# Kernel optimization log

Hardware: AMD Instinct MI355X
Metric: run time of the kernel (lower is better)

The kernel has to match this reference:

```python
import jax, jax.numpy as jnp
import numpy as np

BN_EPS = 1e-5


def _conv1x1(x, W, b):
    # x: (B, Cin, H, W), W: (Cout, Cin), b: (Cout,)
    return jnp.einsum('bchw,oc->bohw', x, W) + b[None, :, None, None]


def _bn(x, gamma, beta, mean, var):
    # inference-mode BatchNorm2d with running stats
    inv = gamma / jnp.sqrt(var + BN_EPS)
    return x * inv[None, :, None, None] + (beta - mean * inv)[None, :, None, None]


def setup_inputs() -> dict:
    key = jax.random.key(0)
    ks = jax.random.split(key, 8)
    B, N, C, H, W = 4, 3, 256, 48, 48
    Ck = C // 2  # key/query/value channels (scale=2)
    s = 0.02
    return {
        'x': jax.random.normal(ks[0], (B, N, C, H, W), jnp.float32),
        # f_key / f_query (shared): conv1x1 + BN
        'Wk': jax.random.normal(ks[1], (Ck, C), jnp.float32) * s,
        'bk': jnp.zeros((Ck,), jnp.float32),
        'gk': jnp.ones((Ck,), jnp.float32),
        'betak': jnp.zeros((Ck,), jnp.float32),
        'mk': jnp.zeros((Ck,), jnp.float32),
        'vk': jnp.ones((Ck,), jnp.float32),
        # f_value
        'Wv': jax.random.normal(ks[2], (Ck, C), jnp.float32) * s,
        'bv': jnp.zeros((Ck,), jnp.float32),
        # f_out
        'Wo': jax.random.normal(ks[3], (C, Ck), jnp.float32) * s,
        'bo': jnp.zeros((C,), jnp.float32),
        # fuse_layer: in = 2*C, out = C
        'Wf': jax.random.normal(ks[4], (C, 2 * C), jnp.float32) * s,
        'bf': jnp.zeros((C,), jnp.float32),
    }


def reference(x, Wk, bk, gk, betak, mk, vk, Wv, bv, Wo, bo, Wf, bf):
    B, N, C, H, W = x.shape  # N == 3
    HW = H * W
    Ck = Wk.shape[0]
    scale = Ck ** (-0.5)

    # Precompute shared key/query and value features for all 3 views
    xf = x.reshape(B * N, C, H, W)
    k_all = _bn(_conv1x1(xf, Wk, bk), gk, betak, mk, vk).reshape(B, N, Ck, HW)
    v_all = _conv1x1(xf, Wv, bv).reshape(B, N, Ck, HW)

    outs = []
    attn_maps = []
    for i in range(3):  # fixed small structural loop over views
        adj_ids = [j for j in range(3) if j != i]
        ref = x[:, i]                          # (B, C, H, W)
        q = k_all[:, i].transpose(0, 2, 1)     # (B, HW, Ck)  f_query == f_key
        matching = jnp.zeros_like(ref)
        for j in adj_ids:
            sim = jnp.einsum('bqc,bck->bqk', q, k_all[:, j]) * scale  # (B, HW, HW)
            attn = jax.nn.softmax(sim, axis=-1)
            ctx = jnp.einsum('bqk,bck->bcq', attn, v_all[:, j])       # (B, Ck, HW)
            ctx = ctx.reshape(B, Ck, H, W)
            matching = matching + _conv1x1(ctx, Wo, bo)
            if i == 0:
                attn_maps.append(attn)
        fuse = _conv1x1(jnp.concatenate([ref, matching], axis=1), Wf, bf)
        outs.append(ref + fuse)

    out = jnp.stack(outs, axis=1)                    # (B, 3, C, H, W)
    attention_maps = jnp.stack(attn_maps, axis=1)    # (B, 2, HW, HW)
    return out, attention_maps
```

## Files before the change

### kernel.cpp

```cpp
#include <hip/hip_runtime.h>

typedef short s8v __attribute__((ext_vector_type(8)));
typedef short s4v __attribute__((ext_vector_type(4)));
typedef float f4v __attribute__((ext_vector_type(4)));
typedef unsigned u32v2 __attribute__((ext_vector_type(2)));
typedef unsigned short u16;

#define MFMA(a,b,c) __builtin_amdgcn_mfma_f32_16x16x32_bf16(a,b,c,0,0,0)

__device__ __forceinline__ float bf2f(u16 x){
  unsigned u = ((unsigned)x) << 16;
  return __builtin_bit_cast(float, u);
}
__device__ __forceinline__ u16 f2bf(float f){
  unsigned u = __builtin_bit_cast(unsigned, f);
  u += 0x7FFFu + ((u >> 16) & 1u);
  return (u16)(u >> 16);
}

__device__ __forceinline__ void gload16(const void* g, void* l){
  __builtin_amdgcn_global_load_lds((const __attribute__((address_space(1))) unsigned*)g,
                                   (__attribute__((address_space(3))) unsigned*)l, 16, 0, 0);
}
__device__ __forceinline__ void nt_store4(float* p, f4v v){
  __builtin_nontemporal_store(v, (f4v*)p);
}

#define CC   256
#define CK   128
#define HW   2304
#define NF   12
#define C2E  0.1275174996992022f
#define OFF_KT   14155776u
#define OFF_V    21233664u
#define OFF_CTX  28311552u
#define OFF_RS   42467328u
#define OFF_PAR  42541056u
#define OFF_WK16 42543104u
#define OFF_WV16 42608640u
#define OFF_WF16 42674176u
#define OFF_WCMB 42936320u

__global__ void cv_weights(const float* __restrict__ Wk, const float* __restrict__ Wv,
                           const float* __restrict__ Wf,
                           u16* __restrict__ Wk16, u16* __restrict__ Wv16, u16* __restrict__ Wf16){
  int i = blockIdx.x*256 + threadIdx.x;
  if (i < 32768){ Wk16[i] = f2bf(Wk[i]); Wv16[i] = f2bf(Wv[i]); }
  Wf16[i] = f2bf(Wf[i]);
}

__global__ void k0_params(const float* __restrict__ bk, const float* __restrict__ gk,
                          const float* __restrict__ betak, const float* __restrict__ mk,
                          const float* __restrict__ vk, const float* __restrict__ Wo,
                          const float* __restrict__ Wf, const float* __restrict__ bo,
                          const float* __restrict__ bfv,
                          float* kscale, float* kbias, float* btot, u16* Wcomb){
  int c = blockIdx.x;
  int o = threadIdx.x;
  float acc = 0.f;
  for(int m=0;m<256;m++)
    acc += Wf[(size_t)o*512 + 256 + m] * Wo[(size_t)m*128 + c];
  Wcomb[(size_t)o*128 + c] = f2bf(acc);
  if (c == 0){
    float a2 = 0.f;
    for(int m=0;m<256;m++)
      a2 += Wf[(size_t)o*512 + 256 + m] * bo[m];
    btot[o] = bfv[o] + 2.0f*a2;
    if (o < 128){
      float inv = gk[o] * rsqrtf(vk[o] + 1e-5f);
      kscale[o] = inv;
      kbias[o]  = betak[o] + (bk[o] - mk[o])*inv;
    }
  }
}

__device__ __forceinline__ void stage_xt(const float* __restrict__ xf, int pb, int tid, char* xt){
  #pragma unroll
  for(int it=0; it<16; ++it){
    int idx = tid + 256*it;
    int c = idx>>4, slot = idx&15;
    f4v v = *(const f4v*)(xf + (size_t)c*HW + pb + slot*4);
    #pragma unroll
    for(int u=0;u<4;u++){
      int p = slot*4+u;
      *(u16*)(xt + p*512 + ((2*c) ^ ((p&7)<<4))) = f2bf(v[u]);
    }
  }
}
__device__ __forceinline__ s8v xt_frag(const char* xt, int r, int kt, int g){
  return *(const s8v*)(xt + r*512 + (((unsigned)(64*kt+16*g)) ^ ((unsigned)(r&7)<<4)));
}

__global__ __launch_bounds__(256) void k1_kv(const float* __restrict__ x, const u16* __restrict__ Wk,
                                             const u16* __restrict__ Wv, const float* __restrict__ bv,
                                             const float* __restrict__ kscale, const float* __restrict__ kbias,
                                             u16* __restrict__ kT, u16* __restrict__ vout){
  int f  = blockIdx.y;
  int pb = blockIdx.x*64;
  int tid = threadIdx.x;
  int w = tid>>6, l = tid&63, s = l&15, g = l>>4;
  __shared__ char xt[32768];
  stage_xt(x + (size_t)f*CC*HW, pb, tid, xt);
  __syncthreads();
  {
    s8v afr[8];
    #pragma unroll
    for(int kt=0;kt<8;kt++) afr[kt] = xt_frag(xt, 16*w+s, kt, g);
    f4v acc[8] = {};
    #pragma unroll
    for(int kt=0;kt<8;kt++){
      #pragma unroll
      for(int nt=0;nt<8;nt++){
        s8v b = *(const s8v*)(Wk + (size_t)(16*nt+s)*CC + 32*kt + 8*g);
        acc[nt] = MFMA(afr[kt], b, acc[nt]);
      }
    }
    u16* kout = kT + (size_t)f*HW*CK;
    int q0 = pb + 16*w;
    #pragma unroll
    for(int nt=0;nt<8;nt++){
      int o = 16*nt + s;
      float sc = kscale[o], bi = kbias[o];
      #pragma unroll
      for(int r=0;r<4;r++){
        int q = q0 + 4*g + r;
        kout[(size_t)q*CK + o] = f2bf(acc[nt][r]*sc + bi);
      }
    }
  }
  {
    s8v afr[2][8];
    #pragma unroll
    for(int mt=0;mt<2;mt++)
      #pragma unroll
      for(int kt=0;kt<8;kt++)
        afr[mt][kt] = *(const s8v*)(Wv + (size_t)(32*w+16*mt+s)*CC + 32*kt + 8*g);
    f4v acc[2][4] = {};
    #pragma unroll
    for(int kt=0;kt<8;kt++){
      #pragma unroll
      for(int nt=0;nt<4;nt++){
        s8v b = xt_frag(xt, 16*nt+s, kt, g);
        #pragma unroll
        for(int mt=0;mt<2;mt++)
          acc[mt][nt] = MFMA(afr[mt][kt], b, acc[mt][nt]);
      }
    }
    u16* vf = vout + (size_t)f*CK*HW;
    #pragma unroll
    for(int mt=0;mt<2;mt++){
      #pragma unroll
      for(int r=0;r<4;r++){
        int o = 32*w + 16*mt + 4*g + r;
        float bvo = bv[o];
        #pragma unroll
        for(int nt=0;nt<4;nt++)
          vf[(size_t)o*HW + pb + 16*nt + s] = f2bf(acc[mt][nt][r] + bvo);
      }
    }
  }
}

__global__ __launch_bounds__(256, 2) void k2_attn(const u16* __restrict__ kT, const u16* __restrict__ v,
                                                  u16* __restrict__ ctxS, float* __restrict__ rowsum_ws){
  int qb  = blockIdx.x;
  int bij = blockIdx.y;
  int b = bij/6, r6 = bij - 6*b, i = r6>>1, jj = r6&1;
  int adj0 = (i==0) ? 1 : 0;
  int adj1 = (i==2) ? 1 : 2;
  int j = jj ? adj1 : adj0;
  int tid = threadIdx.x;
  int w = tid>>6, l = tid&63, s = l&15, g = l>>4;
  int q0 = qb*128 + w*32;

  __shared__ char L[81920];
  char* plw = L + 65536 + w*4096;

  const u16* kTi = kT + (size_t)(b*3+i)*HW*CK;
  const u16* kTj = kT + (size_t)(b*3+j)*HW*CK;
  const u16* vj  = v  + (size_t)(b*3+j)*CK*HW;

  s8v qfr[2][4];
  #pragma unroll
  for(int qf=0;qf<2;qf++)
    #pragma unroll
    for(int kt=0;kt<4;kt++)
      qfr[qf][kt] = *(const s8v*)(kTi + (size_t)(q0+16*qf+s)*CK + 32*kt + 8*g);

  f4v ctx[8][2] = {};
  float psum[2] = {0.f, 0.f};

  auto STAGE = [&](int p0, int buf){
    const char* kbase = (const char*)kTj + (size_t)p0*256;
    const char* vbase = (const char*)vj  + (size_t)p0*2;
    char* lK = L + buf*16384 + w*1024;
    char* lV = L + 32768 + buf*16384 + w*1024;
    #pragma unroll
    for(int it=0; it<4; ++it){
      unsigned Lo = (unsigned)tid*16u + (unsigned)it*4096u;
      unsigned Gs = Lo ^ (((Lo>>8)&7u)<<4);
      gload16(kbase + Gs, lK + it*4096);
      unsigned row = Lo>>7;
      unsigned col = (Lo & 127u) ^ ((row&7u)<<4);
      gload16(vbase + (size_t)row*(HW*2) + col, lV + it*4096);
    }
  };

  STAGE(0, 0);
  __syncthreads();
  int cur = 0;

  for(int pt=0; pt<36; ++pt){
    if (pt < 35) STAGE((pt+1)*64, cur^1);
    const char* lK = L + cur*16384;
    const char* lV = L + 32768 + cur*16384;

    f4v sa[2][4] = {};
    __builtin_amdgcn_s_setprio(1);
    #pragma unroll
    for(int kt=0;kt<4;kt++){
      #pragma unroll
      for(int nt=0;nt<4;nt++){
        unsigned row = (unsigned)(16*nt + s);
        unsigned cb  = ((unsigned)(64*kt + 16*g)) ^ ((row&7u)<<4);
        s8v kfr = *(const s8v*)(lK + row*256 + cb);
        #pragma unroll
        for(int qf=0;qf<2;qf++) sa[qf][nt] = MFMA(kfr, qfr[qf][kt], sa[qf][nt]);
      }
    }
    __builtin_amdgcn_s_setprio(0);
    #pragma unroll
    for(int qf=0;qf<2;qf++){
      #pragma unroll
      for(int nt=0;nt<4;nt++){
        float e0 = exp2f(sa[qf][nt][0]*C2E);
        float e1 = exp2f(sa[qf][nt][1]*C2E);
        float e2 = exp2f(sa[qf][nt][2]*C2E);
        float e3 = exp2f(sa[qf][nt][3]*C2E);
        psum[qf] += (e0+e1)+(e2+e3);
        u32v2 pk;
        pk[0] = (unsigned)f2bf(e0) | ((unsigned)f2bf(e1)<<16);
        pk[1] = (unsigned)f2bf(e2) | ((unsigned)f2bf(e3)<<16);
        unsigned off = ((unsigned)(32*nt + 8*g)) ^ ((unsigned)(s&7)<<4);
        *(u32v2*)(plw + (unsigned)qf*2048u + (unsigned)s*128u + off) = pk;
      }
    }
    s8v pf[2][2];
    #pragma unroll
    for(int qf=0;qf<2;qf++)
      #pragma unroll
      for(int kt=0;kt<2;kt++)
        pf[qf][kt] = *(const s8v*)(plw + (unsigned)qf*2048u + (unsigned)s*128u +
                                   (((unsigned)(64*kt + 16*g)) ^ ((unsigned)(s&7)<<4)));
    __builtin_amdgcn_s_setprio(1);
    #pragma unroll
    for(int kt=0;kt<2;kt++){
      #pragma unroll
      for(int ct=0;ct<8;ct++){
        unsigned row = (unsigned)(16*ct + s);
        unsigned cb  = ((unsigned)(64*kt + 16*g)) ^ ((row&7u)<<4);
        s8v vfr = *(const s8v*)(lV + row*128 + cb);
        #pragma unroll
        for(int qf=0;qf<2;qf++) ctx[ct][qf] = MFMA(vfr, pf[qf][kt], ctx[ct][qf]);
      }
    }
    __builtin_amdgcn_s_setprio(0);
    __syncthreads();
    cur ^= 1;
  }

  float inv[2];
  #pragma unroll
  for(int qf=0;qf<2;qf++){
    float xsum = psum[qf];
    xsum += __shfl_xor(xsum, 16);
    xsum += __shfl_xor(xsum, 32);
    inv[qf] = 1.0f / xsum;
    if (i == 0 && l < 16)
      rowsum_ws[(size_t)(b*2+jj)*HW + q0 + 16*qf + s] = xsum;
  }
  u16* cS = ctxS + (size_t)bij*HW*CK;
  #pragma unroll
  for(int qf=0;qf<2;qf++){
    #pragma unroll
    for(int ct=0;ct<8;ct++){
      s4v pk;
      #pragma unroll
      for(int r=0;r<4;r++) pk[r] = (short)f2bf(ctx[ct][qf][r]*inv[qf]);
      *(s4v*)(cS + (size_t)(q0+16*qf+s)*CK + 16*ct + 4*g) = pk;
    }
  }
}

__global__ __launch_bounds__(256) void k2c_attnmap(const u16* __restrict__ kT,
                                                   const float* __restrict__ rowsum_ws,
                                                   float* __restrict__ attn_out){
  int qb = blockIdx.x;
  int y  = blockIdx.y;
  int plane = y>>1, ph = y&1;
  int b = plane>>1, jj = plane&1, j = jj + 1;
  int tid = threadIdx.x;
  int w = tid>>6, l = tid&63, s = l&15, g = l>>4;
  int q0 = qb*64 + w*16;

  __shared__ char  ldsK[16384];
  __shared__ float ptile[4][16][68];
  __shared__ float inv16[4][16];

  const u16* kTi = kT + (size_t)(b*3)*HW*CK;
  const u16* kTj = kT + (size_t)(b*3+j)*HW*CK;

  s8v qf[4];
  #pragma unroll
  for(int kt=0;kt<4;kt++) qf[kt] = *(const s8v*)(kTi + (size_t)(q0+s)*CK + 32*kt + 8*g);

  {
    f4v rsv = *(const f4v*)(rowsum_ws + (size_t)plane*HW + q0 + 4*g);
    if (s == 0){
      #pragma unroll
      for(int r=0;r<4;r++) inv16[w][4*g+r] = 1.0f / rsv[r];
    }
  }
  __syncthreads();

  float* ao = attn_out + (size_t)plane*HW*HW;

  for(int pt=ph*18; pt<ph*18+18; ++pt){
    int p0 = pt*64;
    {
      const char* kbase = (const char*)kTj + (size_t)p0*256;
      char* lK = (char*)ldsK + w*1024;
      #pragma unroll
      for(int it=0; it<4; ++it){
        unsigned Lo = (unsigned)tid*16u + (unsigned)it*4096u;
        unsigned Gs = Lo ^ (((Lo>>8)&7u)<<4);
        gload16(kbase + Gs, lK + it*4096);
      }
    }
    __syncthreads();

    f4v sa[4] = {};
    #pragma unroll
    for(int kt=0;kt<4;kt++){
      #pragma unroll
      for(int nt=0;nt<4;nt++){
        unsigned row = (unsigned)(16*nt + s);
        unsigned cb  = ((unsigned)(64*kt + 16*g)) ^ ((row&7u)<<4);
        s8v bfr = *(const s8v*)((const char*)ldsK + row*256 + cb);
        sa[nt] = MFMA(qf[kt], bfr, sa[nt]);
      }
    }
    #pragma unroll
    for(int r=0;r<4;r++){
      #pragma unroll
      for(int nt=0;nt<4;nt++)
        ptile[w][4*g+r][16*nt+s] = exp2f(sa[nt][r]*C2E);
    }
    #pragma unroll
    for(int pass=0; pass<4; ++pass){
      int row = 4*pass + g;
      float inv = inv16[w][row];
      f4v val = *(const f4v*)&ptile[w][row][4*s];
      #pragma unroll
      for(int u=0;u<4;u++) val[u] *= inv;
      nt_store4(ao + (size_t)(q0+row)*HW + p0 + 4*s, val);
    }
    __syncthreads();
  }
}

__global__ __launch_bounds__(256) void k3_out(const float* __restrict__ x,
                                              const u16* __restrict__ Wf, const u16* __restrict__ Wcomb,
                                              const float* __restrict__ btot, const u16* __restrict__ ctxS,
                                              float* __restrict__ out){
  int f = blockIdx.y, pb = blockIdx.x*64;
  int tid = threadIdx.x;
  int w = tid>>6, l = tid&63, s = l&15, g = l>>4;
  __shared__ char xt[32768];
  const float* xf = x + (size_t)f*CC*HW;
  stage_xt(xf, pb, tid, xt);
  __syncthreads();
  const u16* cS0 = ctxS + (size_t)(f*2+0)*HW*CK;
  const u16* cS1 = ctxS + (size_t)(f*2+1)*HW*CK;
  f4v acc[4][4] = {};
  #pragma unroll
  for(int kt=0;kt<8;kt++){
    s8v bfr[4];
    #pragma unroll
    for(int nt=0;nt<4;nt++) bfr[nt] = xt_frag(xt, 16*nt+s, kt, g);
    #pragma unroll
    for(int mt=0;mt<4;mt++){
      s8v a = *(const s8v*)(Wf + (size_t)(64*w+16*mt+s)*512 + 32*kt + 8*g);
      #pragma unroll
      for(int nt=0;nt<4;nt++) acc[mt][nt] = MFMA(a, bfr[nt], acc[mt][nt]);
    }
  }
  #pragma unroll
  for(int kt=0;kt<4;kt++){
    s8v b0[4], b1[4];
    #pragma unroll
    for(int nt=0;nt<4;nt++){
      b0[nt] = *(const s8v*)(cS0 + (size_t)(pb+16*nt+s)*CK + 32*kt + 8*g);
      b1[nt] = *(const s8v*)(cS1 + (size_t)(pb+16*nt+s)*CK + 32*kt + 8*g);
    }
    #pragma unroll
    for(int mt=0;mt<4;mt++){
      s8v a = *(const s8v*)(Wcomb + (size_t)(64*w+16*mt+s)*CK + 32*kt + 8*g);
      #pragma unroll
      for(int nt=0;nt<4;nt++){
        acc[mt][nt] = MFMA(a, b0[nt], acc[mt][nt]);
        acc[mt][nt] = MFMA(a, b1[nt], acc[mt][nt]);
      }
    }
  }
  float* of = out + (size_t)f*CC*HW;
  #pragma unroll
  for(int mt=0;mt<4;mt++){
    #pragma unroll
    for(int r=0;r<4;r++){
      int o = 64*w + 16*mt + 4*g + r;
      float bb = btot[o];
      #pragma unroll
      for(int nt=0;nt<4;nt++){
        int p = pb + 16*nt + s;
        of[(size_t)o*HW + p] = acc[mt][nt][r] + bb + xf[(size_t)o*HW + p];
      }
    }
  }
}

extern "C" void kernel_launch(void* const* d_in, const int* in_sizes, int n_in,
                              void* d_out, int out_size, void* d_ws, size_t ws_size,
                              hipStream_t stream) {
  const float* x     = (const float*)d_in[0];
  const float* Wk    = (const float*)d_in[1];
  const float* bk    = (const float*)d_in[2];
  const float* gk    = (const float*)d_in[3];
  const float* betak = (const float*)d_in[4];
  const float* mk    = (const float*)d_in[5];
  const float* vk    = (const float*)d_in[6];
  const float* Wv    = (const float*)d_in[7];
  const float* bv    = (const float*)d_in[8];
  const float* Wo    = (const float*)d_in[9];
  const float* bo    = (const float*)d_in[10];
  const float* Wf    = (const float*)d_in[11];
  const float* bf    = (const float*)d_in[12];
  float* out = (float*)d_out;

  char* ws = (char*)d_ws;
  u16*   kT     = (u16*)(ws + OFF_KT);
  u16*   vv     = (u16*)(ws + OFF_V);
  u16*   ctxS   = (u16*)(ws + OFF_CTX);
  float* rs     = (float*)(ws + OFF_RS);
  float* kscale = (float*)(ws + OFF_PAR);
  float* kbias  = kscale + 128;
  float* btot   = kbias + 128;
  u16*   Wk16   = (u16*)(ws + OFF_WK16);
  u16*   Wv16   = (u16*)(ws + OFF_WV16);
  u16*   Wf16   = (u16*)(ws + OFF_WF16);
  u16*   Wcomb  = (u16*)(ws + OFF_WCMB);

  float* attn = out + (size_t)NF*CC*HW;

  cv_weights<<<dim3(512), dim3(256), 0, stream>>>(Wk, Wv, Wf, Wk16, Wv16, Wf16);
  k0_params<<<dim3(128), dim3(256), 0, stream>>>(bk, gk, betak, mk, vk, Wo, Wf, bo, bf,
                                                 kscale, kbias, btot, Wcomb);
  k1_kv<<<dim3(36,12), dim3(256), 0, stream>>>(x, Wk16, Wv16, bv, kscale, kbias, kT, vv);
  k2_attn<<<dim3(18,24), dim3(256), 0, stream>>>(kT, vv, ctxS, rs);
  k2c_attnmap<<<dim3(36,16), dim3(256), 0, stream>>>(kT, rs, attn);
  k3_out<<<dim3(36,12), dim3(256), 0, stream>>>(x, Wf16, Wcomb, btot, ctxS, out);
}
```

Before: 243.4 us.

## Split attention key range across two blocks and merge partial softmax sums downstream

The attention kernel's key dimension is split in half, doubling the grid from 432 to 864 blocks. Each half writes unnormalized context and partial row sums, and k3_out and the attention-map kernel combine the two halves and normalize. This needs no running max because the softmax has no max subtraction. The weight-conversion kernel is folded into k0_params to save a launch, and the setprio hints are removed. In exchange, ctx workspace traffic doubles and k3_out performs twice as many context MFMAs.

```diff
diff --git a/kernel.cpp b/kernel.cpp
--- a/kernel.cpp
+++ b/kernel.cpp
@@ -31,32 +31,34 @@
 #define HW   2304
 #define NF   12
 #define C2E  0.1275174996992022f
-#define OFF_KT   14155776u
-#define OFF_V    21233664u
-#define OFF_CTX  28311552u
+#define OFF_KT   0u
+#define OFF_V    7077888u
+#define OFF_CTX  14155776u
 #define OFF_RS   42467328u
-#define OFF_PAR  42541056u
-#define OFF_WK16 42543104u
-#define OFF_WV16 42608640u
-#define OFF_WF16 42674176u
-#define OFF_WCMB 42936320u
-
-__global__ void cv_weights(const float* __restrict__ Wk, const float* __restrict__ Wv,
-                           const float* __restrict__ Wf,
-                           u16* __restrict__ Wk16, u16* __restrict__ Wv16, u16* __restrict__ Wf16){
-  int i = blockIdx.x*256 + threadIdx.x;
-  if (i < 32768){ Wk16[i] = f2bf(Wk[i]); Wv16[i] = f2bf(Wv[i]); }
-  Wf16[i] = f2bf(Wf[i]);
-}
-
-__global__ void k0_params(const float* __restrict__ bk, const float* __restrict__ gk,
+#define OFF_PAR  42909696u
+#define OFF_WK16 42911744u
+#define OFF_WV16 42977280u
+#define OFF_WF16 43042816u
+#define OFF_WCMB 43304960u
+
+__global__ void k0_params(const float* __restrict__ Wkf, const float* __restrict__ Wvf,
+                          const float* __restrict__ bk, const float* __restrict__ gk,
                           const float* __restrict__ betak, const float* __restrict__ mk,
                           const float* __restrict__ vk, const float* __restrict__ Wo,
                           const float* __restrict__ Wf, const float* __restrict__ bo,
                           const float* __restrict__ bfv,
+                          u16* __restrict__ Wk16, u16* __restrict__ Wv16, u16* __restrict__ Wf16,
                           float* kscale, float* kbias, float* btot, u16* Wcomb){
   int c = blockIdx.x;
   int o = threadIdx.x;
+  int gid = c*256 + o;
+  Wk16[gid] = f2bf(Wkf[gid]);
+  Wv16[gid] = f2bf(Wvf[gid]);
+  {
+    f4v wf4 = *(const f4v*)(Wf + (size_t)gid*4);
+    #pragma unroll
+    for(int u=0;u<4;u++) Wf16[(size_t)gid*4+u] = f2bf(wf4[u]);
+  }
   float acc = 0.f;
   for(int m=0;m<256;m++)
     acc += Wf[(size_t)o*512 + 256 + m] * Wo[(size_t)m*128 + c];
@@ -162,10 +164,11 @@
 }
 
 __global__ __launch_bounds__(256, 2) void k2_attn(const u16* __restrict__ kT, const u16* __restrict__ v,
-                                                  u16* __restrict__ ctxS, float* __restrict__ rowsum_ws){
+                                                  u16* __restrict__ ctxS, float* __restrict__ rs){
   int qb  = blockIdx.x;
-  int bij = blockIdx.y;
-  int b = bij/6, r6 = bij - 6*b, i = r6>>1, jj = r6&1;
+  int yy  = blockIdx.y;
+  int bij = yy>>1, half = yy&1;
+  int b = bij/6, r6_ = bij - 6*b, i = r6_>>1, jj = r6_&1;
   int adj0 = (i==0) ? 1 : 0;
   int adj1 = (i==2) ? 1 : 2;
   int j = jj ? adj1 : adj0;
@@ -206,17 +209,18 @@
     }
   };
 
-  STAGE(0, 0);
+  int pbase = half*18;
+  STAGE(pbase*64, 0);
   __syncthreads();
   int cur = 0;
 
-  for(int pt=0; pt<36; ++pt){
-    if (pt < 35) STAGE((pt+1)*64, cur^1);
+  for(int pt=0; pt<18; ++pt){
+    int p0 = (pbase + pt)*64;
+    if (pt < 17) STAGE(p0+64, cur^1);
     const char* lK = L + cur*16384;
     const char* lV = L + 32768 + cur*16384;
 
     f4v sa[2][4] = {};
-    __builtin_amdgcn_s_setprio(1);
     #pragma unroll
     for(int kt=0;kt<4;kt++){
       #pragma unroll
@@ -228,7 +232,6 @@
         for(int qf=0;qf<2;qf++) sa[qf][nt] = MFMA(kfr, qfr[qf][kt], sa[qf][nt]);
       }
     }
-    __builtin_amdgcn_s_setprio(0);
     #pragma unroll
     for(int qf=0;qf<2;qf++){
       #pragma unroll
@@ -252,7 +255,6 @@
       for(int kt=0;kt<2;kt++)
         pf[qf][kt] = *(const s8v*)(plw + (unsigned)qf*2048u + (unsigned)s*128u +
                                    (((unsigned)(64*kt + 16*g)) ^ ((unsigned)(s&7)<<4)));
-    __builtin_amdgcn_s_setprio(1);
     #pragma unroll
     for(int kt=0;kt<2;kt++){
       #pragma unroll
@@ -264,36 +266,33 @@
         for(int qf=0;qf<2;qf++) ctx[ct][qf] = MFMA(vfr, pf[qf][kt], ctx[ct][qf]);
       }
     }
-    __builtin_amdgcn_s_setprio(0);
     __syncthreads();
     cur ^= 1;
   }
 
-  float inv[2];
   #pragma unroll
   for(int qf=0;qf<2;qf++){
     float xsum = psum[qf];
     xsum += __shfl_xor(xsum, 16);
     xsum += __shfl_xor(xsum, 32);
-    inv[qf] = 1.0f / xsum;
-    if (i == 0 && l < 16)
-      rowsum_ws[(size_t)(b*2+jj)*HW + q0 + 16*qf + s] = xsum;
-  }
-  u16* cS = ctxS + (size_t)bij*HW*CK;
+    if (l < 16)
+      rs[(size_t)yy*HW + q0 + 16*qf + s] = xsum;
+  }
+  u16* cS = ctxS + (size_t)yy*HW*CK;
   #pragma unroll
   for(int qf=0;qf<2;qf++){
     #pragma unroll
     for(int ct=0;ct<8;ct++){
       s4v pk;
       #pragma unroll
-      for(int r=0;r<4;r++) pk[r] = (short)f2bf(ctx[ct][qf][r]*inv[qf]);
+      for(int r=0;r<4;r++) pk[r] = (short)f2bf(ctx[ct][qf][r]);
       *(s4v*)(cS + (size_t)(q0+16*qf+s)*CK + 16*ct + 4*g) = pk;
     }
   }
 }
 
 __global__ __launch_bounds__(256) void k2c_attnmap(const u16* __restrict__ kT,
-                                                   const float* __restrict__ rowsum_ws,
+                                                   const float* __restrict__ rs,
                                                    float* __restrict__ attn_out){
   int qb = blockIdx.x;
   int y  = blockIdx.y;
@@ -315,10 +314,11 @@
   for(int kt=0;kt<4;kt++) qf[kt] = *(const s8v*)(kTi + (size_t)(q0+s)*CK + 32*kt + 8*g);
 
   {
-    f4v rsv = *(const f4v*)(rowsum_ws + (size_t)plane*HW + q0 + 4*g);
+    f4v ra = *(const f4v*)(rs + (size_t)(12*b+2*jj  )*HW + q0 + 4*g);
+    f4v rb = *(const f4v*)(rs + (size_t)(12*b+2*jj+1)*HW + q0 + 4*g);
     if (s == 0){
       #pragma unroll
-      for(int r=0;r<4;r++) inv16[w][4*g+r] = 1.0f / rsv[r];
+      for(int r=0;r<4;r++) inv16[w][4*g+r] = 1.0f / (ra[r] + rb[r]);
     }
   }
   __syncthreads();
@@ -372,6 +372,7 @@
 __global__ __launch_bounds__(256) void k3_out(const float* __restrict__ x,
                                               const u16* __restrict__ Wf, const u16* __restrict__ Wcomb,
                                               const float* __restrict__ btot, const u16* __restrict__ ctxS,
+                                              const float* __restrict__ rs,
                                               float* __restrict__ out){
   int f = blockIdx.y, pb = blockIdx.x*64;
   int tid = threadIdx.x;
@@ -380,8 +381,6 @@
   const float* xf = x + (size_t)f*CC*HW;
   stage_xt(xf, pb, tid, xt);
   __syncthreads();
-  const u16* cS0 = ctxS + (size_t)(f*2+0)*HW*CK;
-  const u16* cS1 = ctxS + (size_t)(f*2+1)*HW*CK;
   f4v acc[4][4] = {};
   #pragma unroll
   for(int kt=0;kt<8;kt++){
@@ -396,22 +395,42 @@
     }
   }
   #pragma unroll
-  for(int kt=0;kt<4;kt++){
-    s8v b0[4], b1[4];
+  for(int jj=0;jj<2;jj++){
+    const u16* cA = ctxS + (size_t)(4*f+2*jj  )*HW*CK;
+    const u16* cB = ctxS + (size_t)(4*f+2*jj+1)*HW*CK;
+    f4v acc2[4][4] = {};
+    #pragma unroll
+    for(int kt=0;kt<4;kt++){
+      s8v b0[4], b1[4];
+      #pragma unroll
+      for(int nt=0;nt<4;nt++){
+        b0[nt] = *(const s8v*)(cA + (size_t)(pb+16*nt+s)*CK + 32*kt + 8*g);
+        b1[nt] = *(const s8v*)(cB + (size_t)(pb+16*nt+s)*CK + 32*kt + 8*g);
+      }
+      #pragma unroll
+      for(int mt=0;mt<4;mt++){
+        s8v a = *(const s8v*)(Wcomb + (size_t)(64*w+16*mt+s)*CK + 32*kt + 8*g);
+        #pragma unroll
+        for(int nt=0;nt<4;nt++){
+          acc2[mt][nt] = MFMA(a, b0[nt], acc2[mt][nt]);
+          acc2[mt][nt] = MFMA(a, b1[nt], acc2[mt][nt]);
+        }
+      }
+    }
+    const float* rA = rs + (size_t)(4*f+2*jj  )*HW;
+    const float* rB = rs + (size_t)(4*f+2*jj+1)*HW;
+    float invq[4];
     #pragma unroll
     for(int nt=0;nt<4;nt++){
-      b0[nt] = *(const s8v*)(cS0 + (size_t)(pb+16*nt+s)*CK + 32*kt + 8*g);
-      b1[nt] = *(const s8v*)(cS1 + (size_t)(pb+16*nt+s)*CK + 32*kt + 8*g);
-    }
-    #pragma unroll
-    for(int mt=0;mt<4;mt++){
-      s8v a = *(const s8v*)(Wcomb + (size_t)(64*w+16*mt+s)*CK + 32*kt + 8*g);
-      #pragma unroll
-      for(int nt=0;nt<4;nt++){
-        acc[mt][nt] = MFMA(a, b0[nt], acc[mt][nt]);
-        acc[mt][nt] = MFMA(a, b1[nt], acc[mt][nt]);
-      }
-    }
+      int q = pb + 16*nt + s;
+      invq[nt] = 1.0f / (rA[q] + rB[q]);
+    }
+    #pragma unroll
+    for(int mt=0;mt<4;mt++)
+      #pragma unroll
+      for(int nt=0;nt<4;nt++)
+        #pragma unroll
+        for(int r=0;r<4;r++) acc[mt][nt][r] += acc2[mt][nt][r]*invq[nt];
   }
   float* of = out + (size_t)f*CC*HW;
   #pragma unroll
@@ -462,11 +481,10 @@
 
   float* attn = out + (size_t)NF*CC*HW;
 
-  cv_weights<<<dim3(512), dim3(256), 0, stream>>>(Wk, Wv, Wf, Wk16, Wv16, Wf16);
-  k0_params<<<dim3(128), dim3(256), 0, stream>>>(bk, gk, betak, mk, vk, Wo, Wf, bo, bf,
-                                                 kscale, kbias, btot, Wcomb);
+  k0_params<<<dim3(128), dim3(256), 0, stream>>>(Wk, Wv, bk, gk, betak, mk, vk, Wo, Wf, bo, bf,
+                                                 Wk16, Wv16, Wf16, kscale, kbias, btot, Wcomb);
   k1_kv<<<dim3(36,12), dim3(256), 0, stream>>>(x, Wk16, Wv16, bv, kscale, kbias, kT, vv);
-  k2_attn<<<dim3(18,24), dim3(256), 0, stream>>>(kT, vv, ctxS, rs);
+  k2_attn<<<dim3(18,48), dim3(256), 0, stream>>>(kT, vv, ctxS, rs);
   k2c_attnmap<<<dim3(36,16), dim3(256), 0, stream>>>(kT, rs, attn);
-  k3_out<<<dim3(36,12), dim3(256), 0, stream>>>(x, Wf16, Wcomb, btot, ctxS, out);
-}
+  k3_out<<<dim3(36,12), dim3(256), 0, stream>>>(x, Wf16, Wcomb, btot, ctxS, rs, out);
+}
```

Result: faster. 234.0 us (-3.9%).
